# Kernel optimization log

Measured on AMD Instinct MI355X. Metric: run time of the kernel, lower is better.

The kernel has to match this reference:

```python
import jax, jax.numpy as jnp
import numpy as np

N_QUBITS = 16   # downsampled_size**2
N_KERNELS = 2
BSZ = 16        # hardcoded BATCH_SIZE in the repo
INV_SQRT2 = 0.70710678118654752


def ry_mat(theta):
    # RY(t) = [[cos(t/2), -sin(t/2)], [sin(t/2), cos(t/2)]]; theta: scalar or any batch shape
    c = jnp.cos(theta / 2)
    s = jnp.sin(theta / 2)
    m = jnp.stack([jnp.stack([c, -s], -1), jnp.stack([s, c], -1)], -2)
    return m.astype(jnp.complex64)


def rx_mat(theta):
    # RX(t) = [[cos(t/2), -i sin(t/2)], [-i sin(t/2), cos(t/2)]]
    c = jnp.cos(theta / 2).astype(jnp.complex64)
    s = jnp.sin(theta / 2).astype(jnp.complex64)
    return jnp.stack([jnp.stack([c, -1j * s], -1), jnp.stack([-1j * s, c], -1)], -2)


def apply_1q(state, U, w, n):
    # state: (b, 2**n) complex; U: (2,2) or (b,2,2); wire 0 = most significant bit
    b = state.shape[0]
    dl, dr = 1 << w, 1 << (n - 1 - w)
    s = state.reshape(b, dl, 2, dr)
    if U.ndim == 2:
        s = jnp.einsum('ab,xLbR->xLaR', U, s)
    else:
        s = jnp.einsum('xab,xLbR->xLaR', U, s)
    return s.reshape(b, -1)


def apply_cnot(state, c, t, n):
    # flip target axis where control bit == 1
    b = state.shape[0]
    st = state.reshape((b,) + (2,) * n)
    flipped = jnp.flip(st, axis=1 + t)
    mshape = [1] * (n + 1)
    mshape[1 + c] = 2
    ctrl = jnp.arange(2).reshape(mshape)
    st = jnp.where(ctrl == 1, flipped, st)
    return st.reshape(b, -1)


def quantum_model(xd, kernel_params):
    # xd: (b, 16) angles; kernel_params: (n_kernels, 5)
    b = xd.shape[0]
    n = N_QUBITS
    N = 1 << n
    bits = (jnp.arange(N)[:, None] >> jnp.arange(n - 1, -1, -1)[None, :]) & 1
    signs = (1 - 2 * bits).astype(jnp.float32)  # (N, n), PauliZ eigenvalues per wire
    enc = ry_mat(xd)  # (b, 16, 2, 2)
    outs = []
    for k in range(N_KERNELS):
        p = kernel_params[k]
        state = jnp.zeros((b, N), jnp.complex64).at[:, 0].set(1.0)
        # encoder: RY(x_i) on wire i
        for w in range(n):
            state = apply_1q(state, enc[:, w], w, n)
        # QuantumConvolution block (shared 5 trainable angles)
        ry0, ry1, ry2 = ry_mat(p[0]), ry_mat(p[1]), ry_mat(p[2])
        rx0, rx1 = rx_mat(p[3]), rx_mat(p[4])
        for i in range(n - 4):
            state = apply_1q(state, ry0, i, n)
            state = apply_cnot(state, i, i + 3, n)
            state = apply_1q(state, ry1, i + 3, n)
            state = apply_1q(state, ry2, i + 1, n)
            state = apply_cnot(state, i + 1, i + 4, n)
            state = apply_cnot(state, i + 3, i + 1, n)
            state = apply_1q(state, rx0, i + 4, n)
            state = apply_1q(state, rx1, i + 1, n)
        for i in range(n - 4):
            state = apply_cnot(state, i + 1, i, n)
            state = apply_cnot(state, i + 3, i, n)
            state = apply_cnot(state, i + 4, i, n)
        probs = state.real ** 2 + state.imag ** 2  # (b, N)
        expz = probs @ signs                        # (b, n)
        outs.append(expz[:, :-4])                   # drop last 4 wires
    return jnp.concatenate(outs, axis=1)            # (b, n_kernels*(n-4)) = (b, 24)


def setup_inputs() -> dict:
    key = jax.random.key(0)
    ks = jax.random.split(key, 8)
    return {
        'x': jax.random.normal(ks[0], (BSZ, 1, 28, 28), jnp.float32),
        'kernel_params': jax.random.uniform(ks[1], (N_KERNELS, 5), jnp.float32) * (2 * np.pi),
        'fc1_w': jax.random.normal(ks[2], (128, 24), jnp.float32) * 0.1,
        'fc1_b': jnp.zeros((128,), jnp.float32),
        'fc2_w': jax.random.normal(ks[3], (64, 128), jnp.float32) * 0.1,
        'fc2_b': jnp.zeros((64,), jnp.float32),
        'fc3_w': jax.random.normal(ks[4], (4, 64), jnp.float32) * 0.1,
        'fc3_b': jnp.zeros((4,), jnp.float32),
    }


def reference(x, kernel_params, fc1_w, fc1_b, fc2_w, fc2_b, fc3_w, fc3_b):
    b = x.shape[0]
    # AvgPool2d(kernel=7, stride=7): 28x28 -> 4x4, then flatten -> 16 features
    xd = x.reshape(b, 1, 4, 7, 4, 7).mean(axis=(3, 5)).reshape(b, 16)
    feats = quantum_model(xd, kernel_params)       # (b, 24)
    h = jax.nn.relu(feats @ fc1_w.T + fc1_b)
    h = jax.nn.relu(h @ fc2_w.T + fc2_b)
    return h @ fc3_w.T + fc3_b                      # (b, 4)
```

## Files before the change

### kernel.cpp

```cpp
#include <hip/hip_runtime.h>
#include <math.h>

typedef __attribute__((ext_vector_type(2))) float f2;

__device__ __forceinline__ f2 pk_mul_c(f2 cs, f2 a){
  f2 d;
  asm("v_pk_mul_f32 %0, %1, %2 op_sel:[0,0] op_sel_hi:[0,1]"
      : "=v"(d) : "v"(cs), "v"(a));
  return d;
}
__device__ __forceinline__ f2 pk_fma_s(f2 cs, f2 b, f2 t){
  f2 d;
  asm("v_pk_fma_f32 %0, %1, %2, %3 op_sel:[1,0,0] op_sel_hi:[1,1,1]"
      : "=v"(d) : "v"(cs), "v"(b), "v"(t));
  return d;
}
__device__ __forceinline__ f2 pk_fma_ns(f2 cs, f2 b, f2 t){
  f2 d;
  asm("v_pk_fma_f32 %0, %1, %2, %3 op_sel:[1,0,0] op_sel_hi:[1,1,1] neg_lo:[1,0,0] neg_hi:[1,0,0]"
      : "=v"(d) : "v"(cs), "v"(b), "v"(t));
  return d;
}
__device__ __forceinline__ f2 pk_fma_sxn(f2 cs, f2 b, f2 t){
  f2 d;
  asm("v_pk_fma_f32 %0, %1, %2, %3 op_sel:[1,1,0] op_sel_hi:[1,0,1] neg_hi:[0,1,0]"
      : "=v"(d) : "v"(cs), "v"(b), "v"(t));
  return d;
}
__device__ __forceinline__ f2 pk_fma_lo(f2 w, f2 b, f2 t){
  f2 d;
  asm("v_pk_fma_f32 %0, %1, %2, %3 op_sel:[0,0,0] op_sel_hi:[0,1,1]"
      : "=v"(d) : "v"(w), "v"(b), "v"(t));
  return d;
}

template<int B> struct LSH {
  static constexpr int v = (B==7)?0 : (B==8)?1 : (B==2)?2 : (B==1)?3 : (B==0)?4 : 5;
};

template<int PB>
__device__ __forceinline__ float lx(float v){
  if constexpr (PB == 7)
    return __int_as_float(__builtin_amdgcn_update_dpp(
        __float_as_int(v), __float_as_int(v), 0xB1, 0xF, 0xF, false));
  else if constexpr (PB == 8)
    return __int_as_float(__builtin_amdgcn_update_dpp(
        __float_as_int(v), __float_as_int(v), 0x4E, 0xF, 0xF, false));
  else if constexpr (PB == 2)
    return __int_as_float(__builtin_amdgcn_ds_swizzle(__float_as_int(v), 0x101F));
  else if constexpr (PB == 1)
    return __int_as_float(__builtin_amdgcn_ds_swizzle(__float_as_int(v), 0x201F));
  else if constexpr (PB == 0)
    return __int_as_float(__builtin_amdgcn_ds_swizzle(__float_as_int(v), 0x401F));
  else
    return __shfl_xor(v, 32, 64);
}

template<int PB, int CB, bool ISRX>
__device__ __forceinline__ void gate_pass(f2* A, f2 cs, int lane)
{
  if constexpr (PB >= 3 && PB <= 6) {
    constexpr int RM = 1 << (PB - 3);
    bool cl = false;
    if constexpr (CB >= 0 && !(CB >= 3 && CB <= 6))
      cl = (lane >> LSH<CB>::v) & 1;
    #pragma unroll
    for (int r = 0; r < 16; ++r) {
      if (r & RM) continue;
      f2 a0 = A[r], a1 = A[r | RM];
      bool sw;
      if constexpr (CB < 0) sw = false;
      else if constexpr (CB >= 3 && CB <= 6) sw = (r >> (CB - 3)) & 1;
      else sw = cl;
      f2 i0, i1;
      i0.x = sw ? a1.x : a0.x;  i0.y = sw ? a1.y : a0.y;
      i1.x = sw ? a0.x : a1.x;  i1.y = sw ? a0.y : a1.y;
      if constexpr (ISRX) {
        A[r]      = pk_fma_sxn(cs, i1, pk_mul_c(cs, i0));
        A[r | RM] = pk_fma_sxn(cs, i0, pk_mul_c(cs, i1));
      } else {
        A[r]      = pk_fma_ns(cs, i1, pk_mul_c(cs, i0));
        A[r | RM] = pk_fma_s (cs, i0, pk_mul_c(cs, i1));
      }
    }
  } else {
    const int mybit = (lane >> LSH<PB>::v) & 1;
    f2 sv;
    if constexpr (!ISRX) {
      float ssy = mybit ? cs.y : -cs.y;
      sv.x = ssy; sv.y = ssy;
    }
    #pragma unroll
    for (int r = 0; r < 16; ++r) {
      f2 p;
      p.x = lx<PB>(A[r].x);
      p.y = lx<PB>(A[r].y);
      bool sw = false;
      if constexpr (CB >= 3 && CB <= 6) sw = (r >> (CB - 3)) & 1;
      f2 u, v;
      u.x = sw ? p.x : A[r].x;  u.y = sw ? p.y : A[r].y;
      v.x = sw ? A[r].x : p.x;  v.y = sw ? A[r].y : p.y;
      if constexpr (ISRX) A[r] = pk_fma_sxn(cs, v, pk_mul_c(cs, u));
      else                A[r] = pk_fma_lo (sv, v, pk_mul_c(cs, u));
    }
  }
}

template<int LO>
__device__ __forceinline__ void iter_reg(f2* A, int lane,
    f2 cs0, f2 cs1, f2 cs2, f2 csx, f2 cs4)
{
  gate_pass<LO+4, -1,   false>(A, cs0, lane);
  gate_pass<LO+1, LO+4, false>(A, cs1, lane);
  gate_pass<LO+3, -1,   false>(A, cs2, lane);
  gate_pass<LO,   LO+3, true >(A, csx, lane);
  gate_pass<LO+3, LO+1, true >(A, cs4, lane);
}

#define RUN6(A) \
  iter_reg<5>(A, lane, cs0,cs1,cs2,csx,cs4); \
  iter_reg<4>(A, lane, cs0,cs1,cs2,csx,cs4); \
  iter_reg<3>(A, lane, cs0,cs1,cs2,csx,cs4); \
  iter_reg<2>(A, lane, cs0,cs1,cs2,csx,cs4); \
  iter_reg<1>(A, lane, cs0,cs1,cs2,csx,cs4); \
  iter_reg<0>(A, lane, cs0,cs1,cs2,csx,cs4);

__device__ __forceinline__ float wave_sum(float v){
  v += lx<7>(v);
  v += lx<8>(v);
  v += lx<2>(v);
  v += lx<1>(v);
  v += lx<0>(v);
  v += __shfl_xor(v, 32, 64);
  return v;
}

__global__ __launch_bounds__(256) void sim_kernel(
    const float* __restrict__ x, const float* __restrict__ kp,
    float* __restrict__ pacc)
{
  __shared__ __align__(16) float lds[8368];

  const int tid = threadIdx.x, wv = tid >> 6, lane = tid & 63;
  const int gw = blockIdx.x * 4 + wv;
  const int pair = gw >> 6;
  const int chunk = gw & 63;
  const int b = pair & 15, k = pair >> 4;

  f2*    P    = (f2*)&lds[wv * 2048];
  float* angw = &lds[8192 + wv * 32];
  float* stg  = &lds[8320];

  {
    int a = lane >> 2, q = lane & 3;
    int ii = a >> 2, jj = a & 3;
    const float* xb = x + b*784 + ii*7*28 + jj*7;
    const float* r0 = xb + q*28;
    float s = r0[0]+r0[1]+r0[2]+r0[3]+r0[4]+r0[5]+r0[6];
    if (q < 3){
      const float* r1 = xb + (q+4)*28;
      s += r1[0]+r1[1]+r1[2]+r1[3]+r1[4]+r1[5]+r1[6];
    }
    s += __shfl_xor(s, 1, 64);
    s += __shfl_xor(s, 2, 64);
    float ang = s * (1.0f/49.0f) * 0.5f;
    if (q == 0){ angw[a*2] = cosf(ang); angw[a*2+1] = sinf(ang); }
  }

  const float* p5 = kp + k*5;
  f2 cs0, cs1, cs2, csx, cs4;
  cs0.x = cosf(p5[0]*0.5f); cs0.y = sinf(p5[0]*0.5f);
  cs1.x = cosf(p5[1]*0.5f); cs1.y = sinf(p5[1]*0.5f);
  cs2.x = cosf(p5[2]*0.5f); cs2.y = sinf(p5[2]*0.5f);
  csx.x = cosf(p5[3]*0.5f); csx.y = sinf(p5[3]*0.5f);
  cs4.x = cosf(p5[4]*0.5f); cs4.y = sinf(p5[4]*0.5f);

  __threadfence_block();

  f2 A[16];

  {
    float lp = 1.f;
    lp *= ((lane>>5)&1) ? angw[1]  : angw[0];
    lp *= ((lane>>1)&1) ? angw[3]  : angw[2];
    lp *= ( lane    &1) ? angw[5]  : angw[4];
    lp *= ((lane>>2)&1) ? angw[15] : angw[14];
    lp *= ((lane>>3)&1) ? angw[17] : angw[16];
    lp *= ((lane>>4)&1) ? angw[19] : angw[18];
    float c3 = angw[6],  s3 = angw[7];
    float c4w= angw[8],  s4w= angw[9];
    float c5 = angw[10], s5 = angw[11];
    float c6 = angw[12], s6 = angw[13];
    #pragma unroll
    for (int r = 0; r < 16; ++r){
      float rp = ((r&8)? s3:c3) * ((r&4)? s4w:c4w) * ((r&2)? s5:c5) * ((r&1)? s6:c6);
      A[r].x = lp * rp; A[r].y = 0.f;
    }
  }
  RUN6(A);

  #pragma unroll
  for (int r = 0; r < 16; ++r) P[(r << 6) | lane] = A[r];
  __threadfence_block();
  {
    int jc = (((lane>>5)&1) << 2) | (((lane>>1)&1) << 1) | (lane & 1);
    int h0 = (chunk << 4) | (jc << 1);
    int r0_ = (h0 >> 3) & 15;
    int l0_ = ((h0>>7)&1) | (((h0>>8)&1)<<1) | (((h0>>2)&1)<<2)
            | (((h0>>1)&1)<<3) | ((h0&1)<<4) | (((h0>>9)&1)<<5);
    f2 ps0 = P[(r0_ << 6) | l0_];
    f2 ps1 = P[(r0_ << 6) | l0_ | 16];

    float c10 = angw[20], s10 = angw[21];
    float c11 = angw[22], s11 = angw[23];
    float c12 = angw[24], s12 = angw[25];
    float preL = 1.f;
    preL *= ((lane>>2)&1) ? angw[27] : angw[26];
    preL *= ((lane>>3)&1) ? angw[29] : angw[28];
    preL *= ((lane>>4)&1) ? angw[31] : angw[30];
    #pragma unroll
    for (int r = 0; r < 16; ++r){
      float f = preL * (((r&4)? s10:c10) * ((r&2)? s11:c11) * ((r&1)? s12:c12));
      f2 v = (r & 8) ? ps1 : ps0;
      A[r].x = v.x * f; A[r].y = v.y * f;
    }
  }

  RUN6(A);

  float out12[12];
  {
    int idx_hi = (chunk << 10)
      | (((lane>>5)&1) << 9) | (((lane>>1)&1) << 8) | ((lane & 1) << 7)
      | (((lane>>2)&1) << 2) | (((lane>>3)&1) << 1) | ((lane>>4)&1);
    float p[16];
    #pragma unroll
    for (int r = 0; r < 16; ++r) p[r] = A[r].x*A[r].x + A[r].y*A[r].y;
    #pragma unroll
    for (int w = 0; w < 12; ++w){
      float s = 0.f;
      #pragma unroll
      for (int r = 0; r < 16; ++r)
        s += (__popc((r << 3) & (27 << (11 - w))) & 1) ? -p[r] : p[r];
      s = (__popc(idx_hi & (27 << (11 - w))) & 1) ? -s : s;
      out12[w] = wave_sum(s);
    }
  }

  if (lane == 0){
    #pragma unroll
    for (int w = 0; w < 12; ++w) stg[wv*12 + w] = out12[w];
  }
  __syncthreads();
  if (wv == 0 && lane < 12){
    float t = stg[lane] + stg[12+lane] + stg[24+lane] + stg[36+lane];
    pacc[blockIdx.x*12 + lane] = t;
  }
}

__global__ __launch_bounds__(256) void mlp_kernel(
    const float* __restrict__ pacc,
    const float* __restrict__ w1, const float* __restrict__ b1,
    const float* __restrict__ w2, const float* __restrict__ b2,
    const float* __restrict__ w3, const float* __restrict__ b3,
    float* __restrict__ out)
{
  __shared__ __align__(16) float feats[24];
  __shared__ __align__(16) float h1[128];
  __shared__ __align__(16) float h2[64];
  const int tid = threadIdx.x, b = blockIdx.x;

  {
    int f = tid >> 3, part = tid & 7;
    if (f < 24){
      int kk = (f >= 12) ? 1 : 0, w = f - kk*12;
      int pair = kk*16 + b;
      const float* base = pacc + pair*16*12 + w;
      float s = base[part*12] + base[(part+8)*12];
      s += __shfl_xor(s, 1, 64);
      s += __shfl_xor(s, 2, 64);
      s += __shfl_xor(s, 4, 64);
      if (part == 0) feats[f] = s;
    }
  }
  __syncthreads();

  if (tid < 128){
    const float4* wr = (const float4*)(w1 + tid*24);
    const float4* fr = (const float4*)feats;
    float s = b1[tid];
    #pragma unroll
    for (int q = 0; q < 6; ++q){
      float4 a = fr[q], ww = wr[q];
      s += a.x*ww.x + a.y*ww.y + a.z*ww.z + a.w*ww.w;
    }
    h1[tid] = fmaxf(s, 0.f);
  }
  __syncthreads();
  if (tid < 64){
    const float4* wr = (const float4*)(w2 + tid*128);
    const float4* hr = (const float4*)h1;
    float s = b2[tid];
    #pragma unroll
    for (int q = 0; q < 32; ++q){
      float4 a = hr[q], ww = wr[q];
      s += a.x*ww.x + a.y*ww.y + a.z*ww.z + a.w*ww.w;
    }
    h2[tid] = fmaxf(s, 0.f);
  }
  __syncthreads();
  if (tid < 4){
    const float4* wr = (const float4*)(w3 + tid*64);
    const float4* hr = (const float4*)h2;
    float s = b3[tid];
    #pragma unroll
    for (int q = 0; q < 16; ++q){
      float4 a = hr[q], ww = wr[q];
      s += a.x*ww.x + a.y*ww.y + a.z*ww.z + a.w*ww.w;
    }
    out[b*4 + tid] = s;
  }
}

extern "C" void kernel_launch(void* const* d_in, const int* in_sizes, int n_in,
                              void* d_out, int out_size, void* d_ws, size_t ws_size,
                              hipStream_t stream) {
  const float* x  = (const float*)d_in[0];
  const float* kp = (const float*)d_in[1];
  const float* w1 = (const float*)d_in[2];
  const float* b1 = (const float*)d_in[3];
  const float* w2 = (const float*)d_in[4];
  const float* b2 = (const float*)d_in[5];
  const float* w3 = (const float*)d_in[6];
  const float* b3 = (const float*)d_in[7];
  float* out  = (float*)d_out;
  float* pacc = (float*)d_ws;

  sim_kernel<<<512, 256, 0, stream>>>(x, kp, pacc);
  mlp_kernel<<<16, 256, 0, stream>>>(pacc, w1, b1, w2, b2, w3, b3, out);
}
```

Measured before the change: 89.55 us.

## Fuse MLP into sim kernel via flag sync, share first-half state per block

The separate MLP launch is folded into the simulation kernel. Each block publishes its partial sums together with a release-stored magic flag, and the last chunk-block of each batch element spins on those flags and then runs the MLP. The redundant first-half state evolution, previously repeated by all four waves of a block, is now done by one wave and shared through a smaller LDS buffer. The PauliZ expectation reduction is also replaced by a butterfly of sums and differences. Risks: the flags are never cleared between calls, so a later call can pass its spin-wait early and read stale partials. The spin-wait also assumes the producer blocks are co-resident or already finished.

```diff
diff --git a/kernel.cpp b/kernel.cpp
--- a/kernel.cpp
+++ b/kernel.cpp
@@ -135,73 +135,83 @@
   return v;
 }
 
+#define FLAG_MAGIC 0x5CA1AB1Eu
+
 __global__ __launch_bounds__(256) void sim_kernel(
     const float* __restrict__ x, const float* __restrict__ kp,
-    float* __restrict__ pacc)
+    const float* __restrict__ w1, const float* __restrict__ b1,
+    const float* __restrict__ w2, const float* __restrict__ b2,
+    const float* __restrict__ w3, const float* __restrict__ b3,
+    float* __restrict__ pacc,
+    float* __restrict__ out)
 {
-  __shared__ __align__(16) float lds[8368];
+  __shared__ __align__(16) float lds[2048 + 32 + 12 + 48];
+  f2*    P    = (f2*)lds;
+  float* angw = lds + 2048;
+  float* csk  = lds + 2080;
+  float* stg  = lds + 2092;
 
   const int tid = threadIdx.x, wv = tid >> 6, lane = tid & 63;
-  const int gw = blockIdx.x * 4 + wv;
-  const int pair = gw >> 6;
-  const int chunk = gw & 63;
-  const int b = pair & 15, k = pair >> 4;
-
-  f2*    P    = (f2*)&lds[wv * 2048];
-  float* angw = &lds[8192 + wv * 32];
-  float* stg  = &lds[8320];
-
-  {
-    int a = lane >> 2, q = lane & 3;
-    int ii = a >> 2, jj = a & 3;
-    const float* xb = x + b*784 + ii*7*28 + jj*7;
-    const float* r0 = xb + q*28;
-    float s = r0[0]+r0[1]+r0[2]+r0[3]+r0[4]+r0[5]+r0[6];
-    if (q < 3){
-      const float* r1 = xb + (q+4)*28;
-      s += r1[0]+r1[1]+r1[2]+r1[3]+r1[4]+r1[5]+r1[6];
-    }
-    s += __shfl_xor(s, 1, 64);
-    s += __shfl_xor(s, 2, 64);
-    float ang = s * (1.0f/49.0f) * 0.5f;
-    if (q == 0){ angw[a*2] = cosf(ang); angw[a*2+1] = sinf(ang); }
-  }
-
-  const float* p5 = kp + k*5;
-  f2 cs0, cs1, cs2, csx, cs4;
-  cs0.x = cosf(p5[0]*0.5f); cs0.y = sinf(p5[0]*0.5f);
-  cs1.x = cosf(p5[1]*0.5f); cs1.y = sinf(p5[1]*0.5f);
-  cs2.x = cosf(p5[2]*0.5f); cs2.y = sinf(p5[2]*0.5f);
-  csx.x = cosf(p5[3]*0.5f); csx.y = sinf(p5[3]*0.5f);
-  cs4.x = cosf(p5[4]*0.5f); cs4.y = sinf(p5[4]*0.5f);
-
-  __threadfence_block();
+  const int pair  = blockIdx.x >> 4;
+  const int chunk = ((blockIdx.x & 15) << 2) | wv;
+  const int k = pair >> 4;
+  const int lw = blockIdx.x & 3;
 
   f2 A[16];
 
-  {
-    float lp = 1.f;
-    lp *= ((lane>>5)&1) ? angw[1]  : angw[0];
-    lp *= ((lane>>1)&1) ? angw[3]  : angw[2];
-    lp *= ( lane    &1) ? angw[5]  : angw[4];
-    lp *= ((lane>>2)&1) ? angw[15] : angw[14];
-    lp *= ((lane>>3)&1) ? angw[17] : angw[16];
-    lp *= ((lane>>4)&1) ? angw[19] : angw[18];
-    float c3 = angw[6],  s3 = angw[7];
-    float c4w= angw[8],  s4w= angw[9];
-    float c5 = angw[10], s5 = angw[11];
-    float c6 = angw[12], s6 = angw[13];
-    #pragma unroll
-    for (int r = 0; r < 16; ++r){
-      float rp = ((r&8)? s3:c3) * ((r&4)? s4w:c4w) * ((r&2)? s5:c5) * ((r&1)? s6:c6);
-      A[r].x = lp * rp; A[r].y = 0.f;
-    }
-  }
-  RUN6(A);
-
-  #pragma unroll
-  for (int r = 0; r < 16; ++r) P[(r << 6) | lane] = A[r];
-  __threadfence_block();
+  if (wv == lw){
+    {
+      int a = lane >> 2, q = lane & 3;
+      int ii = a >> 2, jj = a & 3;
+      const float* xb = x + (pair & 15)*784 + ii*7*28 + jj*7;
+      const float* r0 = xb + q*28;
+      float s = r0[0]+r0[1]+r0[2]+r0[3]+r0[4]+r0[5]+r0[6];
+      if (q < 3){
+        const float* r1 = xb + (q+4)*28;
+        s += r1[0]+r1[1]+r1[2]+r1[3]+r1[4]+r1[5]+r1[6];
+      }
+      s += __shfl_xor(s, 1, 64);
+      s += __shfl_xor(s, 2, 64);
+      float ang = s * (1.0f/49.0f) * 0.5f;
+      if (q == 0){ angw[a*2] = cosf(ang); angw[a*2+1] = sinf(ang); }
+    }
+    if (lane < 5){
+      float a = kp[k*5 + lane] * 0.5f;
+      csk[lane*2]   = cosf(a);
+      csk[lane*2+1] = sinf(a);
+    }
+    __threadfence_block();
+
+    f2 cs0 = ((f2*)csk)[0], cs1 = ((f2*)csk)[1], cs2 = ((f2*)csk)[2],
+       csx = ((f2*)csk)[3], cs4 = ((f2*)csk)[4];
+
+    {
+      float lp = 1.f;
+      lp *= ((lane>>5)&1) ? angw[1]  : angw[0];
+      lp *= ((lane>>1)&1) ? angw[3]  : angw[2];
+      lp *= ( lane    &1) ? angw[5]  : angw[4];
+      lp *= ((lane>>2)&1) ? angw[15] : angw[14];
+      lp *= ((lane>>3)&1) ? angw[17] : angw[16];
+      lp *= ((lane>>4)&1) ? angw[19] : angw[18];
+      float c3 = angw[6],  s3 = angw[7];
+      float c4w= angw[8],  s4w= angw[9];
+      float c5 = angw[10], s5 = angw[11];
+      float c6 = angw[12], s6 = angw[13];
+      #pragma unroll
+      for (int r = 0; r < 16; ++r){
+        float rp = ((r&8)? s3:c3) * ((r&4)? s4w:c4w) * ((r&2)? s5:c5) * ((r&1)? s6:c6);
+        A[r].x = lp * rp; A[r].y = 0.f;
+      }
+    }
+    RUN6(A);
+
+    #pragma unroll
+    for (int r = 0; r < 16; ++r) P[(r << 6) | lane] = A[r];
+  }
+  __syncthreads();
+
+  f2 cs0 = ((f2*)csk)[0], cs1 = ((f2*)csk)[1], cs2 = ((f2*)csk)[2],
+     csx = ((f2*)csk)[3], cs4 = ((f2*)csk)[4];
   {
     int jc = (((lane>>5)&1) << 2) | (((lane>>1)&1) << 1) | (lane & 1);
     int h0 = (chunk << 4) | (jc << 1);
@@ -233,92 +243,114 @@
     int idx_hi = (chunk << 10)
       | (((lane>>5)&1) << 9) | (((lane>>1)&1) << 8) | ((lane & 1) << 7)
       | (((lane>>2)&1) << 2) | (((lane>>3)&1) << 1) | ((lane>>4)&1);
-    float p[16];
-    #pragma unroll
-    for (int r = 0; r < 16; ++r) p[r] = A[r].x*A[r].x + A[r].y*A[r].y;
+    float p0[16];
+    #pragma unroll
+    for (int r = 0; r < 16; ++r) p0[r] = A[r].x*A[r].x + A[r].y*A[r].y;
+    float e0[8], d0[8];
+    #pragma unroll
+    for (int i = 0; i < 8; ++i){ e0[i] = p0[2*i] + p0[2*i+1]; d0[i] = p0[2*i] - p0[2*i+1]; }
+    float ee[4], ed[4], de[4], dd[4];
+    #pragma unroll
+    for (int j = 0; j < 4; ++j){
+      ee[j] = e0[2*j] + e0[2*j+1];  ed[j] = e0[2*j] - e0[2*j+1];
+      de[j] = d0[2*j] + d0[2*j+1];  dd[j] = d0[2*j] - d0[2*j+1];
+    }
+    float rT  = (ee[0]+ee[1]) + (ee[2]+ee[3]);
+    float r5  = (ee[0]+ee[1]) - (ee[2]+ee[3]);
+    float r6  = (ee[0]-ee[1]) - (ee[2]-ee[3]);
+    float r7  = (ed[0]-ed[1]) + (ed[2]-ed[3]);
+    float r8  = (dd[0]+dd[1]) - (dd[2]+dd[3]);
+    float r9  = (de[0]-de[1]) - (de[2]-de[3]);
+    float r11 = (dd[0]+dd[1]) + (dd[2]+dd[3]);
+    float rsum[12] = {rT,rT,rT,rT,rT, r5, r6, r7, r8, r9, r7, r11};
     #pragma unroll
     for (int w = 0; w < 12; ++w){
-      float s = 0.f;
+      float s = (__popc(idx_hi & (27 << (11 - w))) & 1) ? -rsum[w] : rsum[w];
+      out12[w] = wave_sum(s);
+    }
+  }
+
+  if (lane == 0){
+    #pragma unroll
+    for (int w = 0; w < 12; ++w) stg[wv*12 + w] = out12[w];
+  }
+  __syncthreads();
+  if (wv == 0){
+    if (lane < 12){
+      float t = stg[lane] + stg[12+lane] + stg[24+lane] + stg[36+lane];
+      pacc[blockIdx.x*16 + lane] = t;
+    }
+    __threadfence();
+    if (lane == 0)
+      __hip_atomic_store((unsigned*)(pacc + blockIdx.x*16 + 12), FLAG_MAGIC,
+                         __ATOMIC_RELEASE, __HIP_MEMORY_SCOPE_AGENT);
+  }
+
+  if ((blockIdx.x >= 256) && ((blockIdx.x & 15) == 15)){
+    const int bb = pair & 15;
+    if (tid < 32){
+      int kk = tid >> 4, cb = tid & 15;
+      const unsigned* fp =
+          (const unsigned*)(pacc + (((kk*16 + bb)*16 + cb)*16 + 12));
+      while (__hip_atomic_load(fp, __ATOMIC_RELAXED, __HIP_MEMORY_SCOPE_AGENT)
+             != FLAG_MAGIC)
+        __builtin_amdgcn_s_sleep(2);
+      __threadfence();
+    }
+    __syncthreads();
+
+    float* feats = lds;
+    float* h1    = lds + 32;
+    float* h2    = lds + 160;
+
+    {
+      int f = tid >> 3, part = tid & 7;
+      if (f < 24){
+        int kk = (f >= 12) ? 1 : 0, w = f - kk*12;
+        const float* base = pacc + (kk*16 + bb)*256 + w;
+        float s = base[part*16] + base[(part+8)*16];
+        s += __shfl_xor(s, 1, 64);
+        s += __shfl_xor(s, 2, 64);
+        s += __shfl_xor(s, 4, 64);
+        if (part == 0) feats[f] = s;
+      }
+    }
+    __syncthreads();
+    if (tid < 128){
+      const float4* wr = (const float4*)(w1 + tid*24);
+      const float4* fr = (const float4*)feats;
+      float s = b1[tid];
       #pragma unroll
-      for (int r = 0; r < 16; ++r)
-        s += (__popc((r << 3) & (27 << (11 - w))) & 1) ? -p[r] : p[r];
-      s = (__popc(idx_hi & (27 << (11 - w))) & 1) ? -s : s;
-      out12[w] = wave_sum(s);
-    }
-  }
-
-  if (lane == 0){
-    #pragma unroll
-    for (int w = 0; w < 12; ++w) stg[wv*12 + w] = out12[w];
-  }
-  __syncthreads();
-  if (wv == 0 && lane < 12){
-    float t = stg[lane] + stg[12+lane] + stg[24+lane] + stg[36+lane];
-    pacc[blockIdx.x*12 + lane] = t;
-  }
-}
-
-__global__ __launch_bounds__(256) void mlp_kernel(
-    const float* __restrict__ pacc,
-    const float* __restrict__ w1, const float* __restrict__ b1,
-    const float* __restrict__ w2, const float* __restrict__ b2,
-    const float* __restrict__ w3, const float* __restrict__ b3,
-    float* __restrict__ out)
-{
-  __shared__ __align__(16) float feats[24];
-  __shared__ __align__(16) float h1[128];
-  __shared__ __align__(16) float h2[64];
-  const int tid = threadIdx.x, b = blockIdx.x;
-
-  {
-    int f = tid >> 3, part = tid & 7;
-    if (f < 24){
-      int kk = (f >= 12) ? 1 : 0, w = f - kk*12;
-      int pair = kk*16 + b;
-      const float* base = pacc + pair*16*12 + w;
-      float s = base[part*12] + base[(part+8)*12];
-      s += __shfl_xor(s, 1, 64);
-      s += __shfl_xor(s, 2, 64);
-      s += __shfl_xor(s, 4, 64);
-      if (part == 0) feats[f] = s;
-    }
-  }
-  __syncthreads();
-
-  if (tid < 128){
-    const float4* wr = (const float4*)(w1 + tid*24);
-    const float4* fr = (const float4*)feats;
-    float s = b1[tid];
-    #pragma unroll
-    for (int q = 0; q < 6; ++q){
-      float4 a = fr[q], ww = wr[q];
-      s += a.x*ww.x + a.y*ww.y + a.z*ww.z + a.w*ww.w;
-    }
-    h1[tid] = fmaxf(s, 0.f);
-  }
-  __syncthreads();
-  if (tid < 64){
-    const float4* wr = (const float4*)(w2 + tid*128);
-    const float4* hr = (const float4*)h1;
-    float s = b2[tid];
-    #pragma unroll
-    for (int q = 0; q < 32; ++q){
-      float4 a = hr[q], ww = wr[q];
-      s += a.x*ww.x + a.y*ww.y + a.z*ww.z + a.w*ww.w;
-    }
-    h2[tid] = fmaxf(s, 0.f);
-  }
-  __syncthreads();
-  if (tid < 4){
-    const float4* wr = (const float4*)(w3 + tid*64);
-    const float4* hr = (const float4*)h2;
-    float s = b3[tid];
-    #pragma unroll
-    for (int q = 0; q < 16; ++q){
-      float4 a = hr[q], ww = wr[q];
-      s += a.x*ww.x + a.y*ww.y + a.z*ww.z + a.w*ww.w;
-    }
-    out[b*4 + tid] = s;
+      for (int q = 0; q < 6; ++q){
+        float4 a = fr[q], ww = wr[q];
+        s += a.x*ww.x + a.y*ww.y + a.z*ww.z + a.w*ww.w;
+      }
+      h1[tid] = fmaxf(s, 0.f);
+    }
+    __syncthreads();
+    if (tid < 64){
+      const float4* wr = (const float4*)(w2 + tid*128);
+      const float4* hr = (const float4*)h1;
+      float s = b2[tid];
+      #pragma unroll
+      for (int q = 0; q < 32; ++q){
+        float4 a = hr[q], ww = wr[q];
+        s += a.x*ww.x + a.y*ww.y + a.z*ww.z + a.w*ww.w;
+      }
+      h2[tid] = fmaxf(s, 0.f);
+    }
+    __syncthreads();
+    if (tid < 4){
+      const float4* wr = (const float4*)(w3 + tid*64);
+      const float4* hr = (const float4*)h2;
+      float s = b3[tid];
+      #pragma unroll
+      for (int q = 0; q < 16; ++q){
+        float4 a = hr[q], ww = wr[q];
+        s += a.x*ww.x + a.y*ww.y + a.z*ww.z + a.w*ww.w;
+      }
+      out[bb*4 + tid] = s;
+    }
   }
 }
 
@@ -336,6 +368,5 @@
   float* out  = (float*)d_out;
   float* pacc = (float*)d_ws;
 
-  sim_kernel<<<512, 256, 0, stream>>>(x, kp, pacc);
-  mlp_kernel<<<16, 256, 0, stream>>>(pacc, w1, b1, w2, b2, w3, b3, out);
-}
+  sim_kernel<<<512, 256, 0, stream>>>(x, kp, w1, b1, w2, b2, w3, b3, pacc, out);
+}
```

Measured after the change: 95.36 us. +6.5%, slower.
